# Optimization experiments

Measured on AMD Instinct MI355X. Metric: run time of the kernel, lower is better.

## Reference

```python
import jax, jax.numpy as jnp
import numpy as np

N_LAYERS = 4
HID = 64
N_NODES = 50000
N_EDGES = 800000
N_GRAPHS = 256
NUM_ATOM = 100
NUM_BOND = 4
BN_EPS = 1e-5
GATE_EPS = 1e-6


def _batch_norm(x, gamma, beta):
    # training-mode BatchNorm1d over the node/edge dimension
    mu = jnp.mean(x, axis=0)
    var = jnp.var(x, axis=0)
    return gamma * (x - mu) * jax.lax.rsqrt(var + BN_EPS) + beta


def setup_inputs() -> dict:
    key = jax.random.key(0)
    ks = jax.random.split(key, 12)
    h = jax.random.randint(ks[0], (N_NODES,), 0, NUM_ATOM)
    e = jax.random.randint(ks[1], (N_EDGES,), 0, NUM_BOND)
    src = jax.random.randint(ks[2], (N_EDGES,), 0, N_NODES)
    dst = jax.random.randint(ks[3], (N_EDGES,), 0, N_NODES)
    graph_ids = jnp.sort(jax.random.randint(ks[4], (N_NODES,), 0, N_GRAPHS))
    node_emb = jax.random.normal(ks[5], (NUM_ATOM, HID), dtype=jnp.float32) * 0.1
    edge_emb = jax.random.normal(ks[6], (NUM_BOND, HID), dtype=jnp.float32) * 0.1
    bn_h_gamma = jnp.ones((N_LAYERS, HID), jnp.float32)
    bn_h_beta = jnp.zeros((N_LAYERS, HID), jnp.float32)
    bn_e_gamma = jnp.ones((N_LAYERS, HID), jnp.float32)
    bn_e_beta = jnp.zeros((N_LAYERS, HID), jnp.float32)
    W1 = jax.random.normal(ks[7], (HID, HID // 2), dtype=jnp.float32) * (1.0 / np.sqrt(HID))
    b1 = jnp.zeros((HID // 2,), jnp.float32)
    W2 = jax.random.normal(ks[8], (HID // 2, HID // 4), dtype=jnp.float32) * (1.0 / np.sqrt(HID // 2))
    b2 = jnp.zeros((HID // 4,), jnp.float32)
    W3 = jax.random.normal(ks[9], (HID // 4, 1), dtype=jnp.float32) * (1.0 / np.sqrt(HID // 4))
    b3 = jnp.zeros((1,), jnp.float32)
    return {"h": h, "e": e, "src": src, "dst": dst, "graph_ids": graph_ids,
            "node_emb": node_emb, "edge_emb": edge_emb,
            "bn_h_gamma": bn_h_gamma, "bn_h_beta": bn_h_beta,
            "bn_e_gamma": bn_e_gamma, "bn_e_beta": bn_e_beta,
            "W1": W1, "b1": b1, "W2": W2, "b2": b2, "W3": W3, "b3": b3}


def reference(h, e, src, dst, graph_ids, node_emb, edge_emb,
              bn_h_gamma, bn_h_beta, bn_e_gamma, bn_e_beta,
              W1, b1, W2, b2, W3, b3):
    hf = node_emb[h]          # [N, HID] node encoder
    ef = edge_emb[e]          # [E, HID] edge encoder
    ones_e = jnp.ones((N_EDGES,), hf.dtype)
    deg = jax.ops.segment_sum(ones_e, dst, num_segments=N_NODES)
    norm = jax.lax.rsqrt(jnp.maximum(deg, 1.0))[:, None]  # deg^-0.5, clamp(min=1)
    for l in range(N_LAYERS):
        h_in, e_in = hf, ef
        e_new = hf[src] + hf[dst] + ef            # gather: edge gate pre-activation
        sigma = jax.nn.sigmoid(e_new)
        hn = hf * norm
        msg = jax.ops.segment_sum(sigma * hn[src], dst, num_segments=N_NODES)
        den = jax.ops.segment_sum(sigma, dst, num_segments=N_NODES)
        h_new = (hn + msg / (den + GATE_EPS)) * norm
        h_new = _batch_norm(h_new, bn_h_gamma[l], bn_h_beta[l])
        e_new = _batch_norm(e_new, bn_e_gamma[l], bn_e_beta[l])
        hf = h_in + jax.nn.relu(h_new)            # residual
        ef = e_in + jax.nn.relu(e_new)
    # per-graph mean pooling (dgl.mean_nodes over the batched graph)
    ones_n = jnp.ones((N_NODES,), hf.dtype)
    counts = jax.ops.segment_sum(ones_n, graph_ids, num_segments=N_GRAPHS)
    hg = jax.ops.segment_sum(hf, graph_ids, num_segments=N_GRAPHS)
    hg = hg / jnp.maximum(counts, 1.0)[:, None]   # [G, HID]
    x = jax.nn.relu(hg @ W1 + b1)
    x = jax.nn.relu(x @ W2 + b2)
    return x @ W3 + b3                            # [G, 1]
```

## Files before the change

### kernel.cpp

```cpp
#include <hip/hip_runtime.h>
#include <math.h>

#define N_NODES 50000
#define N_EDGES 800000
#define HID 64
#define N_GRAPHS 256
#define BN_EPS 1e-5f
#define GATE_EPS 1e-6f

static inline size_t align256(size_t x) { return (x + 255) & ~(size_t)255; }


__global__ void k_zero(int* __restrict__ p, int n) {
    for (int i = blockIdx.x * blockDim.x + threadIdx.x; i < n; i += gridDim.x * blockDim.x)
        p[i] = 0;
}

__global__ void k_deg(const int* __restrict__ dst, int* __restrict__ deg) {
    for (int i = blockIdx.x * blockDim.x + threadIdx.x; i < N_EDGES; i += gridDim.x * blockDim.x)
        atomicAdd(&deg[dst[i]], 1);
}

__global__ void k_norm(const int* __restrict__ deg, float* __restrict__ norm) {
    int i = blockIdx.x * blockDim.x + threadIdx.x;
    if (i < N_NODES) norm[i] = 1.0f / sqrtf(fmaxf((float)deg[i], 1.0f));
}

__global__ void k_scan1(const int* __restrict__ deg, int* __restrict__ start,
                        int* __restrict__ blksum) {
    __shared__ int s[256];
    int t = threadIdx.x;
    int i = blockIdx.x * 256 + t;
    int v = (i < N_NODES) ? deg[i] : 0;
    s[t] = v;
    __syncthreads();
    for (int off = 1; off < 256; off <<= 1) {
        int x = (t >= off) ? s[t - off] : 0;
        __syncthreads();
        s[t] += x;
        __syncthreads();
    }
    if (i < N_NODES) start[i] = s[t] - v;
    if (t == 255) blksum[blockIdx.x] = s[255];
}

__global__ void k_scan2(int* __restrict__ blksum, int nb) {
    __shared__ int s[256];
    int t = threadIdx.x;
    int v = (t < nb) ? blksum[t] : 0;
    s[t] = v;
    __syncthreads();
    for (int off = 1; off < 256; off <<= 1) {
        int x = (t >= off) ? s[t - off] : 0;
        __syncthreads();
        s[t] += x;
        __syncthreads();
    }
    if (t < nb) blksum[t] = s[t] - v;
}

__global__ void k_scan3(int* __restrict__ start, const int* __restrict__ blksum,
                        int* __restrict__ cursor) {
    int i = blockIdx.x * 256 + threadIdx.x;
    if (i < N_NODES) {
        int v = start[i] + blksum[blockIdx.x];
        start[i] = v;
        cursor[i] = v;
    }
    if (blockIdx.x == 0 && threadIdx.x == 0) start[N_NODES] = N_EDGES;
}

__global__ void k_scatter(const int* __restrict__ dst, const int* __restrict__ src,
                          const int* __restrict__ etype, const float* __restrict__ norm,
                          int* __restrict__ cursor, int2* __restrict__ edge_meta) {
    for (int i = blockIdx.x * blockDim.x + threadIdx.x; i < N_EDGES; i += gridDim.x * blockDim.x) {
        int p = atomicAdd(&cursor[dst[i]], 1);
        int s = src[i];
        edge_meta[p] = make_int2(s | (etype[i] << 24), __float_as_int(norm[s]));
    }
}

__global__ __launch_bounds__(256) void k_embed(const int* __restrict__ h,
                                               const float* __restrict__ node_emb,
                                               float4* __restrict__ hf4) {
    const int total4 = N_NODES * (HID / 4);
    for (int i = blockIdx.x * blockDim.x + threadIdx.x; i < total4; i += gridDim.x * blockDim.x) {
        int n = i >> 4, c4 = i & 15;
        hf4[i] = ((const float4*)node_emb)[h[n] * (HID / 4) + c4];
    }
}

template <int MODE>
__global__ __launch_bounds__(256, 4) void k_edge(
    const int* __restrict__ start, const int2* __restrict__ edge_meta,
    const float* __restrict__ edge_emb,
    float* __restrict__ ef,
    const float* __restrict__ hf_old, const float* __restrict__ hf_new,
    const float* __restrict__ norm, float* __restrict__ h_new,
    const float* __restrict__ stats_prev, const float* __restrict__ gamma_prev,
    const float* __restrict__ beta_prev,
    float* __restrict__ stats_e_out, float* __restrict__ stats_h_out) {
    const int lane = threadIdx.x & 63;
    const int wid = __builtin_amdgcn_readfirstlane(blockIdx.x * 4 + (threadIdx.x >> 6));
    const int n0 = wid * 4;

    __shared__ float s_emb[4 * HID];
    if (MODE <= 1) {
        for (int i = threadIdx.x; i < 4 * HID; i += blockDim.x) s_emb[i] = edge_emb[i];
        __syncthreads();
    }
    float a_prev = 0.f, c_prev = 0.f;
    if (MODE >= 1) {
        float s1 = stats_prev[lane], s2 = stats_prev[HID + lane];
        float mu = s1 * (1.0f / N_EDGES);
        float var = s2 * (1.0f / N_EDGES) - mu * mu;
        float rstd = 1.0f / sqrtf(var + BN_EPS);
        a_prev = gamma_prev[lane] * rstd;
        c_prev = beta_prev[lane] - mu * a_prev;
    }

    int jbeg[4], len[4];
    float hnn[4], hon[4], amsg[4], aden[4];
    int maxlen = 0;
#pragma unroll
    for (int k = 0; k < 4; ++k) {
        jbeg[k] = start[n0 + k];
        len[k] = start[n0 + k + 1] - jbeg[k];
        maxlen = max(maxlen, len[k]);
        hnn[k] = hf_new[(n0 + k) * HID + lane];
        hon[k] = (MODE >= 1) ? hf_old[(n0 + k) * HID + lane] : 0.f;
        amsg[k] = 0.f;
        aden[k] = 0.f;
    }

    auto eidx = [&](int k, int it) {
        int itc = min(it, max(len[k] - 1, 0));
        return min(jbeg[k] + itc, N_EDGES - 1);
    };

    float sum_e = 0.f, sumsq_e = 0.f, sum_h = 0.f, sumsq_h = 0.f;
    if (maxlen > 0) {
        int2 mt[4];
        float efp[4];
#pragma unroll
        for (int k = 0; k < 4; ++k) {
            const int j0 = eidx(k, 0);
            mt[k] = edge_meta[j0];
            efp[k] = (MODE >= 2) ? ef[(size_t)j0 * HID + lane] : 0.f;
        }
        for (int it = 0; it < maxlen; ++it) {
            int sg[4];
            float hs[4], ho[4];
#pragma unroll
            for (int k = 0; k < 4; ++k) {
                sg[k] = mt[k].x & 0xFFFFFF;
                hs[k] = hf_new[sg[k] * HID + lane];
                ho[k] = (MODE >= 1) ? hf_old[sg[k] * HID + lane] : 0.f;
            }
            const int itn = (it + 1 < maxlen) ? it + 1 : it;
            int2 mtn[4];
            float efn[4];
#pragma unroll
            for (int k = 0; k < 4; ++k) {
                const int jn = eidx(k, itn);
                mtn[k] = edge_meta[jn];
                efn[k] = (MODE >= 2) ? ef[(size_t)jn * HID + lane] : 0.f;
            }
#pragma unroll
            for (int k = 0; k < 4; ++k) {
                const bool act = it < len[k];
                float efv;
                if (MODE == 0) {
                    efv = s_emb[(mt[k].x >> 24) * HID + lane];
                } else if (MODE == 1) {
                    const float ef0 = s_emb[(mt[k].x >> 24) * HID + lane];
                    const float ep = ho[k] + hon[k] + ef0;
                    efv = ef0 + fmaxf(a_prev * ep + c_prev, 0.f);
                    if (act) ef[(size_t)(jbeg[k] + it) * HID + lane] = efv;
                } else {
                    const float ep = ho[k] + hon[k] + efp[k];
                    efv = efp[k] + fmaxf(a_prev * ep + c_prev, 0.f);
                    if (MODE == 2) {
                        if (act) ef[(size_t)(jbeg[k] + it) * HID + lane] = efv;
                    }
                }
                const float en = hs[k] + hnn[k] + efv;
                const float sgm = 1.0f / (1.0f + __expf(-en));
                if (act) {
                    amsg[k] += sgm * hs[k] * __int_as_float(mt[k].y);
                    aden[k] += sgm;
                    if (MODE != 3) { sum_e += en; sumsq_e += en * en; }
                }
            }
#pragma unroll
            for (int k = 0; k < 4; ++k) { mt[k] = mtn[k]; efp[k] = efn[k]; }
        }
    }

#pragma unroll
    for (int k = 0; k < 4; ++k) {
        const float nm = norm[n0 + k];
        const float hval = (hnn[k] * nm + amsg[k] / (aden[k] + GATE_EPS)) * nm;
        h_new[(n0 + k) * HID + lane] = hval;
        sum_h += hval;
        sumsq_h += hval * hval;
    }

    __shared__ float sred[4][256];
    sred[0][threadIdx.x] = sum_e;
    sred[1][threadIdx.x] = sumsq_e;
    sred[2][threadIdx.x] = sum_h;
    sred[3][threadIdx.x] = sumsq_h;
    __syncthreads();
    if (threadIdx.x < 64) {
        const int t = threadIdx.x;
        if (MODE != 3) {
            float t1 = sred[0][t] + sred[0][t + 64] + sred[0][t + 128] + sred[0][t + 192];
            float t2 = sred[1][t] + sred[1][t + 64] + sred[1][t + 128] + sred[1][t + 192];
            atomicAdd(&stats_e_out[t], t1);
            atomicAdd(&stats_e_out[HID + t], t2);
        }
        float t3 = sred[2][t] + sred[2][t + 64] + sred[2][t + 128] + sred[2][t + 192];
        float t4 = sred[3][t] + sred[3][t + 64] + sred[3][t + 128] + sred[3][t + 192];
        atomicAdd(&stats_h_out[t], t3);
        atomicAdd(&stats_h_out[HID + t], t4);
    }
}

__global__ __launch_bounds__(256) void k_hupd(
    const float4* __restrict__ hf_in, const float4* __restrict__ h_new,
    const float* __restrict__ stats, const float* __restrict__ gamma,
    const float* __restrict__ beta, float4* __restrict__ hf_out) {
    const int tid = blockIdx.x * blockDim.x + threadIdx.x;
    const int c0 = (tid & 15) * 4;
    float a[4], c[4];
#pragma unroll
    for (int k = 0; k < 4; ++k) {
        int ch = c0 + k;
        float mu = stats[ch] * (1.0f / N_NODES);
        float var = stats[HID + ch] * (1.0f / N_NODES) - mu * mu;
        float rstd = 1.0f / sqrtf(var + BN_EPS);
        a[k] = gamma[ch] * rstd;
        c[k] = beta[ch] - mu * a[k];
    }
    const int total4 = N_NODES * (HID / 4);
    for (int i = tid; i < total4; i += gridDim.x * blockDim.x) {
        float4 hi = hf_in[i], hn = h_new[i], o;
        o.x = hi.x + fmaxf(a[0] * hn.x + c[0], 0.f);
        o.y = hi.y + fmaxf(a[1] * hn.y + c[1], 0.f);
        o.z = hi.z + fmaxf(a[2] * hn.z + c[2], 0.f);
        o.w = hi.w + fmaxf(a[3] * hn.w + c[3], 0.f);
        hf_out[i] = o;
    }
}

__global__ __launch_bounds__(256) void k_poolmlp(
    const float* __restrict__ hf, const int* __restrict__ graph_ids,
    const float* __restrict__ W1, const float* __restrict__ b1,
    const float* __restrict__ W2, const float* __restrict__ b2,
    const float* __restrict__ W3, const float* __restrict__ b3,
    float* __restrict__ out) {
    const int g = blockIdx.x;
    int a = 0, b = N_NODES;
    while (a < b) { int m = (a + b) >> 1; if (graph_ids[m] < g) a = m + 1; else b = m; }
    const int lo = a;
    b = N_NODES;
    while (a < b) { int m = (a + b) >> 1; if (graph_ids[m] < g + 1) a = m + 1; else b = m; }
    const int hi = a;

    const int lane = threadIdx.x & 63, w = threadIdx.x >> 6;
    float acc = 0.f;
    for (int n = lo + w; n < hi; n += 4) acc += hf[n * HID + lane];
    __shared__ float sred[256];
    __shared__ float sh[64], sx1[32], sx2[16];
    sred[threadIdx.x] = acc;
    __syncthreads();
    if (threadIdx.x < 64) {
        float tot = sred[lane] + sred[lane + 64] + sred[lane + 128] + sred[lane + 192];
        sh[lane] = tot / fmaxf((float)(hi - lo), 1.0f);
    }
    __syncthreads();
    const int t = threadIdx.x;
    if (t < 32) {
        float s = b1[t];
        for (int c = 0; c < 64; ++c) s += sh[c] * W1[c * 32 + t];
        sx1[t] = fmaxf(s, 0.f);
    }
    __syncthreads();
    if (t < 16) {
        float s = b2[t];
        for (int k = 0; k < 32; ++k) s += sx1[k] * W2[k * 16 + t];
        sx2[t] = fmaxf(s, 0.f);
    }
    __syncthreads();
    if (t == 0) {
        float s = b3[0];
        for (int k = 0; k < 16; ++k) s += sx2[k] * W3[k];
        out[g] = s;
    }
}


extern "C" void kernel_launch(void* const* d_in, const int* in_sizes, int n_in,
                              void* d_out, int out_size, void* d_ws, size_t ws_size,
                              hipStream_t stream) {
    const int* h_idx      = (const int*)d_in[0];
    const int* e_idx      = (const int*)d_in[1];
    const int* src        = (const int*)d_in[2];
    const int* dst        = (const int*)d_in[3];
    const int* graph_ids  = (const int*)d_in[4];
    const float* node_emb = (const float*)d_in[5];
    const float* edge_emb = (const float*)d_in[6];
    const float* bnh_g    = (const float*)d_in[7];
    const float* bnh_b    = (const float*)d_in[8];
    const float* bne_g    = (const float*)d_in[9];
    const float* bne_b    = (const float*)d_in[10];
    const float* W1       = (const float*)d_in[11];
    const float* b1       = (const float*)d_in[12];
    const float* W2       = (const float*)d_in[13];
    const float* b2       = (const float*)d_in[14];
    const float* W3       = (const float*)d_in[15];
    const float* b3       = (const float*)d_in[16];
    float* out = (float*)d_out;

    char* w = (char*)d_ws;
    size_t off = 0;
    auto alloc = [&](size_t bytes) -> void* {
        void* p = w + off;
        off = align256(off + bytes);
        return p;
    };
    float* ef        = (float*)alloc((size_t)N_EDGES * HID * 4);
    float* hfA       = (float*)alloc((size_t)N_NODES * HID * 4);
    float* hfB       = (float*)alloc((size_t)N_NODES * HID * 4);
    float* h_new     = (float*)alloc((size_t)N_NODES * HID * 4);
    float* norm      = (float*)alloc((size_t)N_NODES * 4);
    int2*  edge_meta = (int2*)alloc((size_t)N_EDGES * 8);
    int*   start     = (int*)alloc((size_t)(N_NODES + 1) * 4);
    int*   cursor    = (int*)alloc((size_t)N_NODES * 4);
    int*   blksum    = (int*)alloc(256 * 4);
    size_t zoff = off;
    int*   deg       = (int*)alloc((size_t)N_NODES * 4);
    float* stats_e   = (float*)alloc(4 * 2 * HID * 4);
    float* stats_h   = (float*)alloc(4 * 2 * HID * 4);
    int zero_elems = (int)((off - zoff) / 4);
    int* zbase = (int*)(w + zoff);

    const int NB_SCAN = (N_NODES + 255) / 256;

    k_zero<<<64, 256, 0, stream>>>(zbase, zero_elems);
    k_deg<<<1024, 256, 0, stream>>>(dst, deg);
    k_norm<<<NB_SCAN, 256, 0, stream>>>(deg, norm);
    k_scan1<<<NB_SCAN, 256, 0, stream>>>(deg, start, blksum);
    k_scan2<<<1, 256, 0, stream>>>(blksum, NB_SCAN);
    k_scan3<<<NB_SCAN, 256, 0, stream>>>(start, blksum, cursor);
    k_scatter<<<1024, 256, 0, stream>>>(dst, src, e_idx, norm, cursor, edge_meta);
    k_embed<<<512, 256, 0, stream>>>(h_idx, node_emb, (float4*)hfA);

    const int EG = N_NODES / 16;
    const int NG = 512;

    k_edge<0><<<EG, 256, 0, stream>>>(start, edge_meta, edge_emb, ef,
        nullptr, hfA, norm, h_new, nullptr, nullptr, nullptr,
        stats_e + 0 * 128, stats_h + 0 * 128);
    k_hupd<<<NG, 256, 0, stream>>>((const float4*)hfA, (const float4*)h_new,
        stats_h + 0 * 128, bnh_g + 0 * HID, bnh_b + 0 * HID, (float4*)hfB);

    k_edge<1><<<EG, 256, 0, stream>>>(start, edge_meta, edge_emb, ef,
        hfA, hfB, norm, h_new, stats_e + 0 * 128, bne_g + 0 * HID, bne_b + 0 * HID,
        stats_e + 1 * 128, stats_h + 1 * 128);
    k_hupd<<<NG, 256, 0, stream>>>((const float4*)hfB, (const float4*)h_new,
        stats_h + 1 * 128, bnh_g + 1 * HID, bnh_b + 1 * HID, (float4*)hfA);

    k_edge<2><<<EG, 256, 0, stream>>>(start, edge_meta, edge_emb, ef,
        hfB, hfA, norm, h_new, stats_e + 1 * 128, bne_g + 1 * HID, bne_b + 1 * HID,
        stats_e + 2 * 128, stats_h + 2 * 128);
    k_hupd<<<NG, 256, 0, stream>>>((const float4*)hfA, (const float4*)h_new,
        stats_h + 2 * 128, bnh_g + 2 * HID, bnh_b + 2 * HID, (float4*)hfB);

    k_edge<3><<<EG, 256, 0, stream>>>(start, edge_meta, edge_emb, ef,
        hfA, hfB, norm, h_new, stats_e + 2 * 128, bne_g + 2 * HID, bne_b + 2 * HID,
        stats_e + 3 * 128, stats_h + 3 * 128);
    k_hupd<<<NG, 256, 0, stream>>>((const float4*)hfB, (const float4*)h_new,
        stats_h + 3 * 128, bnh_g + 3 * HID, bnh_b + 3 * HID, (float4*)hfA);

    k_poolmlp<<<N_GRAPHS, 256, 0, stream>>>(hfA, graph_ids, W1, b1, W2, b2, W3, b3, out);
}
```

Baseline: 757.9 us.

## Interleave old/new node features into float2 pairs and deepen gather prefetch

Replaces the two ping-pong node feature buffers with one interleaved buffer holding (new, old) per channel. Each neighbor gather then fetches both values in a single 8-byte load instead of two separate 4-byte loads from different arrays. The edge loop is software-pipelined two iterations deep, prefetching metadata and ef two steps ahead and the node pair one step ahead, with a sched_barrier and readfirstlane on the CSR offsets. The cost is that the node buffer doubles in size, so MODE 0 loads unused old values, and register pressure rises from the deeper prefetch.

```diff
diff --git a/kernel.cpp b/kernel.cpp
--- a/kernel.cpp
+++ b/kernel.cpp
@@ -82,11 +82,12 @@
 
 __global__ __launch_bounds__(256) void k_embed(const int* __restrict__ h,
                                                const float* __restrict__ node_emb,
-                                               float4* __restrict__ hf4) {
-    const int total4 = N_NODES * (HID / 4);
-    for (int i = blockIdx.x * blockDim.x + threadIdx.x; i < total4; i += gridDim.x * blockDim.x) {
-        int n = i >> 4, c4 = i & 15;
-        hf4[i] = ((const float4*)node_emb)[h[n] * (HID / 4) + c4];
+                                               float4* __restrict__ pair4) {
+    const int total2 = N_NODES * (HID / 2);
+    for (int i = blockIdx.x * blockDim.x + threadIdx.x; i < total2; i += gridDim.x * blockDim.x) {
+        int n = i >> 5, c2 = i & 31;
+        float2 e = ((const float2*)node_emb)[h[n] * (HID / 2) + c2];
+        pair4[i] = make_float4(e.x, 0.f, e.y, 0.f);
     }
 }
 
@@ -95,7 +96,7 @@
     const int* __restrict__ start, const int2* __restrict__ edge_meta,
     const float* __restrict__ edge_emb,
     float* __restrict__ ef,
-    const float* __restrict__ hf_old, const float* __restrict__ hf_new,
+    const float2* __restrict__ pair,
     const float* __restrict__ norm, float* __restrict__ h_new,
     const float* __restrict__ stats_prev, const float* __restrict__ gamma_prev,
     const float* __restrict__ beta_prev,
@@ -124,76 +125,87 @@
     int maxlen = 0;
 #pragma unroll
     for (int k = 0; k < 4; ++k) {
-        jbeg[k] = start[n0 + k];
-        len[k] = start[n0 + k + 1] - jbeg[k];
+        jbeg[k] = __builtin_amdgcn_readfirstlane(start[n0 + k]);
+        len[k] = __builtin_amdgcn_readfirstlane(start[n0 + k + 1]) - jbeg[k];
         maxlen = max(maxlen, len[k]);
-        hnn[k] = hf_new[(n0 + k) * HID + lane];
-        hon[k] = (MODE >= 1) ? hf_old[(n0 + k) * HID + lane] : 0.f;
+        float2 o = pair[(size_t)(n0 + k) * HID + lane];
+        hnn[k] = o.x;
+        hon[k] = (MODE >= 1) ? o.y : 0.f;
         amsg[k] = 0.f;
         aden[k] = 0.f;
     }
 
-    auto eidx = [&](int k, int it) {
+    auto eslot = [&](int k, int it) {
         int itc = min(it, max(len[k] - 1, 0));
         return min(jbeg[k] + itc, N_EDGES - 1);
     };
 
     float sum_e = 0.f, sumsq_e = 0.f, sum_h = 0.f, sumsq_h = 0.f;
     if (maxlen > 0) {
-        int2 mt[4];
-        float efp[4];
+        int2 mt0[4], mt1[4];
+        float ef0[4], ef1[4];
+        float2 hp0[4];
 #pragma unroll
         for (int k = 0; k < 4; ++k) {
-            const int j0 = eidx(k, 0);
-            mt[k] = edge_meta[j0];
-            efp[k] = (MODE >= 2) ? ef[(size_t)j0 * HID + lane] : 0.f;
+            const int j = eslot(k, 0);
+            mt0[k] = edge_meta[j];
+            ef0[k] = (MODE >= 2) ? ef[(size_t)j * HID + lane] : 0.f;
+        }
+#pragma unroll
+        for (int k = 0; k < 4; ++k)
+            hp0[k] = pair[(size_t)(mt0[k].x & 0xFFFFFF) * HID + lane];
+#pragma unroll
+        for (int k = 0; k < 4; ++k) {
+            const int j = eslot(k, 1);
+            mt1[k] = edge_meta[j];
+            ef1[k] = (MODE >= 2) ? ef[(size_t)j * HID + lane] : 0.f;
         }
         for (int it = 0; it < maxlen; ++it) {
-            int sg[4];
-            float hs[4], ho[4];
+            float2 hp1[4];
+#pragma unroll
+            for (int k = 0; k < 4; ++k)
+                hp1[k] = pair[(size_t)(mt1[k].x & 0xFFFFFF) * HID + lane];
+            int2 mt2[4];
+            float ef2[4];
+            const int itn = (it + 2 < maxlen) ? it + 2 : maxlen - 1;
 #pragma unroll
             for (int k = 0; k < 4; ++k) {
-                sg[k] = mt[k].x & 0xFFFFFF;
-                hs[k] = hf_new[sg[k] * HID + lane];
-                ho[k] = (MODE >= 1) ? hf_old[sg[k] * HID + lane] : 0.f;
+                const int j = eslot(k, itn);
+                mt2[k] = edge_meta[j];
+                ef2[k] = (MODE >= 2) ? ef[(size_t)j * HID + lane] : 0.f;
             }
-            const int itn = (it + 1 < maxlen) ? it + 1 : it;
-            int2 mtn[4];
-            float efn[4];
-#pragma unroll
-            for (int k = 0; k < 4; ++k) {
-                const int jn = eidx(k, itn);
-                mtn[k] = edge_meta[jn];
-                efn[k] = (MODE >= 2) ? ef[(size_t)jn * HID + lane] : 0.f;
-            }
+            __builtin_amdgcn_sched_barrier(0);
 #pragma unroll
             for (int k = 0; k < 4; ++k) {
                 const bool act = it < len[k];
                 float efv;
                 if (MODE == 0) {
-                    efv = s_emb[(mt[k].x >> 24) * HID + lane];
+                    efv = s_emb[(mt0[k].x >> 24) * HID + lane];
                 } else if (MODE == 1) {
-                    const float ef0 = s_emb[(mt[k].x >> 24) * HID + lane];
-                    const float ep = ho[k] + hon[k] + ef0;
-                    efv = ef0 + fmaxf(a_prev * ep + c_prev, 0.f);
+                    const float e0v = s_emb[(mt0[k].x >> 24) * HID + lane];
+                    const float ep = hp0[k].y + hon[k] + e0v;
+                    efv = e0v + fmaxf(a_prev * ep + c_prev, 0.f);
                     if (act) ef[(size_t)(jbeg[k] + it) * HID + lane] = efv;
                 } else {
-                    const float ep = ho[k] + hon[k] + efp[k];
-                    efv = efp[k] + fmaxf(a_prev * ep + c_prev, 0.f);
+                    const float ep = hp0[k].y + hon[k] + ef0[k];
+                    efv = ef0[k] + fmaxf(a_prev * ep + c_prev, 0.f);
                     if (MODE == 2) {
                         if (act) ef[(size_t)(jbeg[k] + it) * HID + lane] = efv;
                     }
                 }
-                const float en = hs[k] + hnn[k] + efv;
+                const float en = hp0[k].x + hnn[k] + efv;
                 const float sgm = 1.0f / (1.0f + __expf(-en));
                 if (act) {
-                    amsg[k] += sgm * hs[k] * __int_as_float(mt[k].y);
+                    amsg[k] += sgm * hp0[k].x * __int_as_float(mt0[k].y);
                     aden[k] += sgm;
                     if (MODE != 3) { sum_e += en; sumsq_e += en * en; }
                 }
             }
 #pragma unroll
-            for (int k = 0; k < 4; ++k) { mt[k] = mtn[k]; efp[k] = efn[k]; }
+            for (int k = 0; k < 4; ++k) {
+                mt0[k] = mt1[k]; ef0[k] = ef1[k]; hp0[k] = hp1[k];
+                mt1[k] = mt2[k]; ef1[k] = ef2[k];
+            }
         }
     }
 
@@ -228,34 +240,33 @@
 }
 
 __global__ __launch_bounds__(256) void k_hupd(
-    const float4* __restrict__ hf_in, const float4* __restrict__ h_new,
+    float4* pair4, const float2* __restrict__ h_new2,
     const float* __restrict__ stats, const float* __restrict__ gamma,
-    const float* __restrict__ beta, float4* __restrict__ hf_out) {
+    const float* __restrict__ beta) {
     const int tid = blockIdx.x * blockDim.x + threadIdx.x;
-    const int c0 = (tid & 15) * 4;
-    float a[4], c[4];
-#pragma unroll
-    for (int k = 0; k < 4; ++k) {
-        int ch = c0 + k;
+    const int cb = (tid & 31) * 2;
+    float a[2], c[2];
+#pragma unroll
+    for (int k = 0; k < 2; ++k) {
+        int ch = cb + k;
         float mu = stats[ch] * (1.0f / N_NODES);
         float var = stats[HID + ch] * (1.0f / N_NODES) - mu * mu;
         float rstd = 1.0f / sqrtf(var + BN_EPS);
         a[k] = gamma[ch] * rstd;
         c[k] = beta[ch] - mu * a[k];
     }
-    const int total4 = N_NODES * (HID / 4);
-    for (int i = tid; i < total4; i += gridDim.x * blockDim.x) {
-        float4 hi = hf_in[i], hn = h_new[i], o;
-        o.x = hi.x + fmaxf(a[0] * hn.x + c[0], 0.f);
-        o.y = hi.y + fmaxf(a[1] * hn.y + c[1], 0.f);
-        o.z = hi.z + fmaxf(a[2] * hn.z + c[2], 0.f);
-        o.w = hi.w + fmaxf(a[3] * hn.w + c[3], 0.f);
-        hf_out[i] = o;
+    const int total2 = N_NODES * (HID / 2);
+    for (int i = tid; i < total2; i += gridDim.x * blockDim.x) {
+        float4 p = pair4[i];
+        float2 hn = h_new2[i];
+        float o0 = p.x + fmaxf(a[0] * hn.x + c[0], 0.f);
+        float o1 = p.z + fmaxf(a[1] * hn.y + c[1], 0.f);
+        pair4[i] = make_float4(o0, p.x, o1, p.z);
     }
 }
 
 __global__ __launch_bounds__(256) void k_poolmlp(
-    const float* __restrict__ hf, const int* __restrict__ graph_ids,
+    const float2* __restrict__ pair, const int* __restrict__ graph_ids,
     const float* __restrict__ W1, const float* __restrict__ b1,
     const float* __restrict__ W2, const float* __restrict__ b2,
     const float* __restrict__ W3, const float* __restrict__ b3,
@@ -270,7 +281,7 @@
 
     const int lane = threadIdx.x & 63, w = threadIdx.x >> 6;
     float acc = 0.f;
-    for (int n = lo + w; n < hi; n += 4) acc += hf[n * HID + lane];
+    for (int n = lo + w; n < hi; n += 4) acc += pair[(size_t)n * HID + lane].x;
     __shared__ float sred[256];
     __shared__ float sh[64], sx1[32], sx2[16];
     sred[threadIdx.x] = acc;
@@ -330,19 +341,18 @@
         off = align256(off + bytes);
         return p;
     };
-    float* ef        = (float*)alloc((size_t)N_EDGES * HID * 4);
-    float* hfA       = (float*)alloc((size_t)N_NODES * HID * 4);
-    float* hfB       = (float*)alloc((size_t)N_NODES * HID * 4);
-    float* h_new     = (float*)alloc((size_t)N_NODES * HID * 4);
-    float* norm      = (float*)alloc((size_t)N_NODES * 4);
-    int2*  edge_meta = (int2*)alloc((size_t)N_EDGES * 8);
-    int*   start     = (int*)alloc((size_t)(N_NODES + 1) * 4);
-    int*   cursor    = (int*)alloc((size_t)N_NODES * 4);
-    int*   blksum    = (int*)alloc(256 * 4);
+    float*  ef        = (float*)alloc((size_t)N_EDGES * HID * 4);
+    float2* pair      = (float2*)alloc((size_t)N_NODES * HID * 8);
+    float*  h_new     = (float*)alloc((size_t)N_NODES * HID * 4);
+    float*  norm      = (float*)alloc((size_t)N_NODES * 4);
+    int2*   edge_meta = (int2*)alloc((size_t)N_EDGES * 8);
+    int*    start     = (int*)alloc((size_t)(N_NODES + 1) * 4);
+    int*    cursor    = (int*)alloc((size_t)N_NODES * 4);
+    int*    blksum    = (int*)alloc(256 * 4);
     size_t zoff = off;
-    int*   deg       = (int*)alloc((size_t)N_NODES * 4);
-    float* stats_e   = (float*)alloc(4 * 2 * HID * 4);
-    float* stats_h   = (float*)alloc(4 * 2 * HID * 4);
+    int*    deg       = (int*)alloc((size_t)N_NODES * 4);
+    float*  stats_e   = (float*)alloc(4 * 2 * HID * 4);
+    float*  stats_h   = (float*)alloc(4 * 2 * HID * 4);
     int zero_elems = (int)((off - zoff) / 4);
     int* zbase = (int*)(w + zoff);
 
@@ -355,34 +365,34 @@
     k_scan2<<<1, 256, 0, stream>>>(blksum, NB_SCAN);
     k_scan3<<<NB_SCAN, 256, 0, stream>>>(start, blksum, cursor);
     k_scatter<<<1024, 256, 0, stream>>>(dst, src, e_idx, norm, cursor, edge_meta);
-    k_embed<<<512, 256, 0, stream>>>(h_idx, node_emb, (float4*)hfA);
+    k_embed<<<512, 256, 0, stream>>>(h_idx, node_emb, (float4*)pair);
 
     const int EG = N_NODES / 16;
     const int NG = 512;
 
     k_edge<0><<<EG, 256, 0, stream>>>(start, edge_meta, edge_emb, ef,
-        nullptr, hfA, norm, h_new, nullptr, nullptr, nullptr,
+        pair, norm, h_new, nullptr, nullptr, nullptr,
         stats_e + 0 * 128, stats_h + 0 * 128);
-    k_hupd<<<NG, 256, 0, stream>>>((const float4*)hfA, (const float4*)h_new,
-        stats_h + 0 * 128, bnh_g + 0 * HID, bnh_b + 0 * HID, (float4*)hfB);
+    k_hupd<<<NG, 256, 0, stream>>>((float4*)pair, (const float2*)h_new,
+        stats_h + 0 * 128, bnh_g + 0 * HID, bnh_b + 0 * HID);
 
     k_edge<1><<<EG, 256, 0, stream>>>(start, edge_meta, edge_emb, ef,
-        hfA, hfB, norm, h_new, stats_e + 0 * 128, bne_g + 0 * HID, bne_b + 0 * HID,
+        pair, norm, h_new, stats_e + 0 * 128, bne_g + 0 * HID, bne_b + 0 * HID,
         stats_e + 1 * 128, stats_h + 1 * 128);
-    k_hupd<<<NG, 256, 0, stream>>>((const float4*)hfB, (const float4*)h_new,
-        stats_h + 1 * 128, bnh_g + 1 * HID, bnh_b + 1 * HID, (float4*)hfA);
+    k_hupd<<<NG, 256, 0, stream>>>((float4*)pair, (const float2*)h_new,
+        stats_h + 1 * 128, bnh_g + 1 * HID, bnh_b + 1 * HID);
 
     k_edge<2><<<EG, 256, 0, stream>>>(start, edge_meta, edge_emb, ef,
-        hfB, hfA, norm, h_new, stats_e + 1 * 128, bne_g + 1 * HID, bne_b + 1 * HID,
+        pair, norm, h_new, stats_e + 1 * 128, bne_g + 1 * HID, bne_b + 1 * HID,
         stats_e + 2 * 128, stats_h + 2 * 128);
-    k_hupd<<<NG, 256, 0, stream>>>((const float4*)hfA, (const float4*)h_new,
-        stats_h + 2 * 128, bnh_g + 2 * HID, bnh_b + 2 * HID, (float4*)hfB);
+    k_hupd<<<NG, 256, 0, stream>>>((float4*)pair, (const float2*)h_new,
+        stats_h + 2 * 128, bnh_g + 2 * HID, bnh_b + 2 * HID);
 
     k_edge<3><<<EG, 256, 0, stream>>>(start, edge_meta, edge_emb, ef,
-        hfA, hfB, norm, h_new, stats_e + 2 * 128, bne_g + 2 * HID, bne_b + 2 * HID,
+        pair, norm, h_new, stats_e + 2 * 128, bne_g + 2 * HID, bne_b + 2 * HID,
         stats_e + 3 * 128, stats_h + 3 * 128);
-    k_hupd<<<NG, 256, 0, stream>>>((const float4*)hfB, (const float4*)h_new,
-        stats_h + 3 * 128, bnh_g + 3 * HID, bnh_b + 3 * HID, (float4*)hfA);
-
-    k_poolmlp<<<N_GRAPHS, 256, 0, stream>>>(hfA, graph_ids, W1, b1, W2, b2, W3, b3, out);
-}
+    k_hupd<<<NG, 256, 0, stream>>>((float4*)pair, (const float2*)h_new,
+        stats_h + 3 * 128, bnh_g + 3 * HID, bnh_b + 3 * HID);
+
+    k_poolmlp<<<N_GRAPHS, 256, 0, stream>>>(pair, graph_ids, W1, b1, W2, b2, W3, b3, out);
+}
```

Result: slower. 775.3 us (+2.3%).
